# Performance work log

Hardware: AMD Instinct MI355X
Metric: run time of the kernel (lower is better)

Reference implementation:

```python
import jax, jax.numpy as jnp
import numpy as np

B, N, CIN, COUT = 8192, 17, 256, 256


def setup_inputs() -> dict:
    key = jax.random.key(0)
    k_x, k_w, k_m, k_a, k_b = jax.random.split(key, 5)
    stdv = 1.0 / np.sqrt(COUT)
    return {
        "x": jax.random.normal(k_x, (B, N, CIN), dtype=jnp.float32),
        # xavier_uniform with gain=1.414 ~ U(-a, a), a = gain*sqrt(6/(fan_in+fan_out))
        "W": jax.random.uniform(k_w, (2, CIN, COUT), dtype=jnp.float32,
                                minval=-1.0, maxval=1.0) * (1.414 * np.sqrt(6.0 / (CIN + COUT))),
        # M initialized to ones in torch; perturb slightly to exercise the math
        "M": 1.0 + 0.1 * jax.random.normal(k_m, (N, COUT), dtype=jnp.float32),
        "adj": jax.random.uniform(k_a, (N, N), dtype=jnp.float32),
        "adj2": jnp.full((N, N), 1e-6, dtype=jnp.float32),
        "bias": jax.random.uniform(k_b, (COUT,), dtype=jnp.float32,
                                   minval=-stdv, maxval=stdv),
    }


def reference(x, W, M, adj, adj2, bias):
    # x: [B, N, Cin], W: [2, Cin, Cout], M: [N, Cout], adj/adj2: [N, N]
    h0 = jnp.einsum("bnc,cd->bnd", x, W[0])  # [B, N, Cout]
    h1 = jnp.einsum("bnc,cd->bnd", x, W[1])  # [B, N, Cout]
    A = adj + adj2
    A = (A.T + A) * 0.5                       # symmetrize
    E = jnp.eye(A.shape[0], dtype=x.dtype)
    out = (jnp.einsum("ij,bjd->bid", A * E, M * h0)
           + jnp.einsum("ij,bjd->bid", A * (1.0 - E), M * h1))
    return out + bias[None, None, :]
```

## Files before the change

### kernel.cpp

```cpp
#include <hip/hip_runtime.h>
#include <hip/hip_bf16.h>

typedef float  f32x4  __attribute__((ext_vector_type(4)));
typedef __bf16 bf16x8 __attribute__((ext_vector_type(8)));
typedef short  s16x8  __attribute__((ext_vector_type(8)));
typedef short  s16x4  __attribute__((ext_vector_type(4)));

__device__ __forceinline__ short f2b(float f) {
  unsigned u = __builtin_bit_cast(unsigned, f);
  u = (u + 0x7fffu + ((u >> 16) & 1u)) >> 16;
  return (short)u;
}
__device__ __forceinline__ float b2f(short s) {
  unsigned u = ((unsigned)(unsigned short)s) << 16;
  return __builtin_bit_cast(float, u);
}
__device__ __forceinline__ s16x4 pack4(f32x4 a) {
  union { s16x4 v; __hip_bfloat162 h[2]; } u;
  u.h[0] = __float22bfloat162_rn(make_float2(a[0], a[1]));
  u.h[1] = __float22bfloat162_rn(make_float2(a[2], a[3]));
  return u.v;
}

__global__ void prep_wt(const float* __restrict__ W, short* __restrict__ Wt) {
  int q = blockIdx.x * blockDim.x + threadIdx.x;
  int mat = q >> 14;
  int rem = q & 16383;
  int d   = rem >> 6;
  int c4  = (rem & 63) << 2;
  const float* src = W + mat * 65536;
  s16x4 o;
  #pragma unroll
  for (int i = 0; i < 4; ++i) o[i] = f2b(src[(c4 + i) * 256 + d]);
  *(s16x4*)&Wt[q << 2] = o;
}

__global__ __launch_bounds__(256)
void fused_mgc(const float* __restrict__ x, const short* __restrict__ Wt,
               const float* __restrict__ M, const float* __restrict__ adj,
               const float* __restrict__ adj2, const float* __restrict__ bias,
               float* __restrict__ out) {
  __shared__ short smem[8976];
  __shared__ float aoff[289];
  __shared__ float diagl[17];

  const int tid  = threadIdx.x;
  const int lane = tid & 63;
  const int wv   = tid >> 6;
  const int m16  = lane & 15;
  const int qd   = lane >> 4;

  const int phys = blockIdx.x;
  const int xcd  = phys & 7;
  const int iseq = phys >> 3;
  const int bt   = xcd * 512 + (iseq >> 1);
  const int ct   = iseq & 1;

  for (int idx = tid; idx < 289; idx += 256) {
    int i = idx / 17, j = idx - i * 17;
    float v = 0.5f * ((adj[i*17+j] + adj2[i*17+j]) + (adj[j*17+i] + adj2[j*17+i]));
    aoff[idx] = (i == j) ? 0.0f : v;
    if (i == j) diagl[i] = adj[i*17+i] + adj2[i*17+i];
  }

  {
    const float* xbase = x + (size_t)bt * 34 * 256;
    const int c4 = (tid & 63) << 2;
    const int r0 = tid >> 6;
    #pragma unroll
    for (int it = 0; it < 9; ++it) {
      int row = r0 + it * 4;
      if (row < 34) {
        f32x4 v = *(const f32x4*)&xbase[row * 256 + c4];
        *(s16x4*)&smem[row * 264 + c4] = pack4(v);
      }
    }
  }

  f32x4 acc[3][4];
  #pragma unroll
  for (int a = 0; a < 3; ++a)
    #pragma unroll
    for (int b = 0; b < 4; ++b) acc[a][b] = (f32x4)0.0f;

  const short* wbase = Wt + (ct * 128 + wv * 32 + m16) * 256;

  __syncthreads();

  int arow[3];
  #pragma unroll
  for (int rf = 0; rf < 3; ++rf) {
    int r = rf * 16 + m16;
    arow[rf] = (r < 34 ? r : 33) * 264;
  }

  #pragma unroll
  for (int ks = 0; ks < 8; ++ks) {
    const int kq = ks * 32 + qd * 8;
    bf16x8 bfr[4];
    #pragma unroll
    for (int mc = 0; mc < 4; ++mc) {
      int mat = mc >> 1, cf = mc & 1;
      s16x8 t = *(const s16x8*)&wbase[mat * 65536 + cf * 4096 + kq];
      bfr[mc] = __builtin_bit_cast(bf16x8, t);
    }
    #pragma unroll
    for (int rf = 0; rf < 3; ++rf) {
      s16x8 t = *(const s16x8*)&smem[arow[rf] + kq];
      bf16x8 af = __builtin_bit_cast(bf16x8, t);
      #pragma unroll
      for (int mc = 0; mc < 4; ++mc)
        acc[rf][mc] = __builtin_amdgcn_mfma_f32_16x16x32_bf16(af, bfr[mc], acc[rf][mc], 0, 0, 0);
    }
  }

  __syncthreads();
  short* sbuf = smem;
  short* gbuf = smem + 4488;

  #pragma unroll
  for (int rf = 0; rf < 3; ++rf) {
    #pragma unroll
    for (int cf = 0; cf < 2; ++cf) {
      int c = wv * 32 + cf * 16 + m16;
      #pragma unroll
      for (int reg = 0; reg < 4; ++reg) {
        int r = rf * 16 + qd * 4 + reg;
        if (r < 34) {
          int n = r % 17;
          float mv = M[n * 256 + ct * 128 + c];
          sbuf[r * 132 + c] = f2b(diagl[n] * mv * acc[rf][cf][reg]);
          gbuf[r * 132 + c] = f2b(mv * acc[rf][2 + cf][reg]);
        }
      }
    }
  }
  __syncthreads();
  const int d7   = tid & 127;
  const int g    = tid >> 7;
  const float bi = bias[ct * 128 + d7];
  {
    int rbase = g * 17;
    float gr[17];
    #pragma unroll
    for (int j = 0; j < 17; ++j) gr[j] = b2f(gbuf[(rbase + j) * 132 + d7]);
    #pragma unroll
    for (int i = 0; i < 17; ++i) {
      float s = b2f(sbuf[(rbase + i) * 132 + d7]) + bi;
      #pragma unroll
      for (int j = 0; j < 17; ++j) s += aoff[i * 17 + j] * gr[j];
      out[((bt * 2 + g) * 17 + i) * 256 + ct * 128 + d7] = s;
    }
  }
}

extern "C" void kernel_launch(void* const* d_in, const int* in_sizes, int n_in,
                              void* d_out, int out_size, void* d_ws, size_t ws_size,
                              hipStream_t stream) {
  const float* x    = (const float*)d_in[0];
  const float* W    = (const float*)d_in[1];
  const float* M    = (const float*)d_in[2];
  const float* adj  = (const float*)d_in[3];
  const float* adj2 = (const float*)d_in[4];
  const float* bias = (const float*)d_in[5];
  float* out = (float*)d_out;
  short* Wt  = (short*)d_ws;

  prep_wt<<<128, 256, 0, stream>>>(W, Wt);
  fused_mgc<<<8192, 256, 0, stream>>>(x, Wt, M, adj, adj2, bias, out);
}
```

Measured before the change: 413.2 us.

## Loop each block over eight batch tiles with register prefetch of next x

Each block now processes eight consecutive batch tiles in a loop, so the grid shrinks by a factor of eight. The next tile's x is prefetched into registers during the current tile's MFMA and epilogue. M and the adjacency setup are staged into shared memory once per block. The aim is to hide global-load latency and amortise per-block setup, at the cost of more registers, fewer resident blocks and extra barriers per tile.

```diff
diff --git a/kernel.cpp b/kernel.cpp
--- a/kernel.cpp
+++ b/kernel.cpp
@@ -40,7 +40,8 @@
                const float* __restrict__ M, const float* __restrict__ adj,
                const float* __restrict__ adj2, const float* __restrict__ bias,
                float* __restrict__ out) {
-  __shared__ short smem[8976];
+  __shared__ short xs[8976];
+  __shared__ float ms[2176];
   __shared__ float aoff[289];
   __shared__ float diagl[17];
 
@@ -50,42 +51,36 @@
   const int m16  = lane & 15;
   const int qd   = lane >> 4;
 
-  const int phys = blockIdx.x;
-  const int xcd  = phys & 7;
-  const int iseq = phys >> 3;
-  const int bt   = xcd * 512 + (iseq >> 1);
-  const int ct   = iseq & 1;
+  const int phys   = blockIdx.x;
+  const int xcd    = phys & 7;
+  const int iseq   = phys >> 3;
+  const int ct     = iseq & 1;
+  const int btbase = (xcd * 64 + (iseq >> 1)) * 8;
 
+  const int c4 = (tid & 63) << 2;
+  const int r0 = tid >> 6;
+
+  f32x4 xp[9];
+  {
+    const float* xb = x + (size_t)btbase * 34 * 256;
+    #pragma unroll
+    for (int it = 0; it < 9; ++it) {
+      int row = r0 + it * 4;
+      if (row < 34) xp[it] = *(const f32x4*)&xb[row * 256 + c4];
+    }
+  }
   for (int idx = tid; idx < 289; idx += 256) {
     int i = idx / 17, j = idx - i * 17;
     float v = 0.5f * ((adj[i*17+j] + adj2[i*17+j]) + (adj[j*17+i] + adj2[j*17+i]));
     aoff[idx] = (i == j) ? 0.0f : v;
     if (i == j) diagl[i] = adj[i*17+i] + adj2[i*17+i];
   }
-
-  {
-    const float* xbase = x + (size_t)bt * 34 * 256;
-    const int c4 = (tid & 63) << 2;
-    const int r0 = tid >> 6;
-    #pragma unroll
-    for (int it = 0; it < 9; ++it) {
-      int row = r0 + it * 4;
-      if (row < 34) {
-        f32x4 v = *(const f32x4*)&xbase[row * 256 + c4];
-        *(s16x4*)&smem[row * 264 + c4] = pack4(v);
-      }
-    }
+  for (int q = tid; q < 544; q += 256) {
+    int n = q >> 5, cq = (q & 31) << 2;
+    *(f32x4*)&ms[n * 128 + cq] = *(const f32x4*)&M[n * 256 + ct * 128 + cq];
   }
 
-  f32x4 acc[3][4];
-  #pragma unroll
-  for (int a = 0; a < 3; ++a)
-    #pragma unroll
-    for (int b = 0; b < 4; ++b) acc[a][b] = (f32x4)0.0f;
-
   const short* wbase = Wt + (ct * 128 + wv * 32 + m16) * 256;
-
-  __syncthreads();
 
   int arow[3];
   #pragma unroll
@@ -94,63 +89,91 @@
     arow[rf] = (r < 34 ? r : 33) * 264;
   }
 
-  #pragma unroll
-  for (int ks = 0; ks < 8; ++ks) {
-    const int kq = ks * 32 + qd * 8;
-    bf16x8 bfr[4];
+  const int d7   = tid & 127;
+  const int g    = tid >> 7;
+  const float bi = bias[ct * 128 + d7];
+
+  for (int t = 0; t < 8; ++t) {
+    const int bt = btbase + t;
+
     #pragma unroll
-    for (int mc = 0; mc < 4; ++mc) {
-      int mat = mc >> 1, cf = mc & 1;
-      s16x8 t = *(const s16x8*)&wbase[mat * 65536 + cf * 4096 + kq];
-      bfr[mc] = __builtin_bit_cast(bf16x8, t);
+    for (int it = 0; it < 9; ++it) {
+      int row = r0 + it * 4;
+      if (row < 34) *(s16x4*)&xs[row * 264 + c4] = pack4(xp[it]);
     }
+    __syncthreads();
+
+    if (t < 7) {
+      const float* xb = x + (size_t)(bt + 1) * 34 * 256;
+      #pragma unroll
+      for (int it = 0; it < 9; ++it) {
+        int row = r0 + it * 4;
+        if (row < 34) xp[it] = *(const f32x4*)&xb[row * 256 + c4];
+      }
+    }
+
+    f32x4 acc[3][4];
+    #pragma unroll
+    for (int a = 0; a < 3; ++a)
+      #pragma unroll
+      for (int b = 0; b < 4; ++b) acc[a][b] = (f32x4)0.0f;
+
+    #pragma unroll
+    for (int ks = 0; ks < 8; ++ks) {
+      const int kq = ks * 32 + qd * 8;
+      bf16x8 bfr[4];
+      #pragma unroll
+      for (int mc = 0; mc < 4; ++mc) {
+        int mat = mc >> 1, cf = mc & 1;
+        s16x8 w = *(const s16x8*)&wbase[mat * 65536 + cf * 4096 + kq];
+        bfr[mc] = __builtin_bit_cast(bf16x8, w);
+      }
+      #pragma unroll
+      for (int rf = 0; rf < 3; ++rf) {
+        s16x8 a8 = *(const s16x8*)&xs[arow[rf] + kq];
+        bf16x8 af = __builtin_bit_cast(bf16x8, a8);
+        #pragma unroll
+        for (int mc = 0; mc < 4; ++mc)
+          acc[rf][mc] = __builtin_amdgcn_mfma_f32_16x16x32_bf16(af, bfr[mc], acc[rf][mc], 0, 0, 0);
+      }
+    }
+    __syncthreads();
+
+    short* sbuf = xs;
+    short* gbuf = xs + 4488;
     #pragma unroll
     for (int rf = 0; rf < 3; ++rf) {
-      s16x8 t = *(const s16x8*)&smem[arow[rf] + kq];
-      bf16x8 af = __builtin_bit_cast(bf16x8, t);
       #pragma unroll
-      for (int mc = 0; mc < 4; ++mc)
-        acc[rf][mc] = __builtin_amdgcn_mfma_f32_16x16x32_bf16(af, bfr[mc], acc[rf][mc], 0, 0, 0);
-    }
-  }
-
-  __syncthreads();
-  short* sbuf = smem;
-  short* gbuf = smem + 4488;
-
-  #pragma unroll
-  for (int rf = 0; rf < 3; ++rf) {
-    #pragma unroll
-    for (int cf = 0; cf < 2; ++cf) {
-      int c = wv * 32 + cf * 16 + m16;
-      #pragma unroll
-      for (int reg = 0; reg < 4; ++reg) {
-        int r = rf * 16 + qd * 4 + reg;
-        if (r < 34) {
-          int n = r % 17;
-          float mv = M[n * 256 + ct * 128 + c];
-          sbuf[r * 132 + c] = f2b(diagl[n] * mv * acc[rf][cf][reg]);
-          gbuf[r * 132 + c] = f2b(mv * acc[rf][2 + cf][reg]);
+      for (int cf = 0; cf < 2; ++cf) {
+        int c = wv * 32 + cf * 16 + m16;
+        #pragma unroll
+        for (int reg = 0; reg < 4; ++reg) {
+          int r = rf * 16 + qd * 4 + reg;
+          if (r < 34) {
+            int n = r - (r >= 17 ? 17 : 0);
+            float mv = ms[n * 128 + c];
+            sbuf[r * 132 + c] = f2b(diagl[n] * mv * acc[rf][cf][reg]);
+            gbuf[r * 132 + c] = f2b(mv * acc[rf][2 + cf][reg]);
+          }
         }
       }
     }
-  }
-  __syncthreads();
-  const int d7   = tid & 127;
-  const int g    = tid >> 7;
-  const float bi = bias[ct * 128 + d7];
-  {
-    int rbase = g * 17;
-    float gr[17];
-    #pragma unroll
-    for (int j = 0; j < 17; ++j) gr[j] = b2f(gbuf[(rbase + j) * 132 + d7]);
-    #pragma unroll
-    for (int i = 0; i < 17; ++i) {
-      float s = b2f(sbuf[(rbase + i) * 132 + d7]) + bi;
+    __syncthreads();
+
+    {
+      int rbase = g * 17;
+      float gr[17];
       #pragma unroll
-      for (int j = 0; j < 17; ++j) s += aoff[i * 17 + j] * gr[j];
-      out[((bt * 2 + g) * 17 + i) * 256 + ct * 128 + d7] = s;
+      for (int j = 0; j < 17; ++j) gr[j] = b2f(gbuf[(rbase + j) * 132 + d7]);
+      #pragma unroll
+      for (int i = 0; i < 17; ++i) {
+        float s = b2f(sbuf[(rbase + i) * 132 + d7]) + bi;
+        #pragma unroll
+        for (int j = 0; j < 17; ++j) s += aoff[i * 17 + j] * gr[j];
+        out[((bt * 2 + g) * 17 + i) * 256 + ct * 128 + d7] = s;
+      }
     }
+    __syncthreads();
   }
 }
 
@@ -167,5 +190,5 @@
   short* Wt  = (short*)d_ws;
 
   prep_wt<<<128, 256, 0, stream>>>(W, Wt);
-  fused_mgc<<<8192, 256, 0, stream>>>(x, Wt, M, adj, adj2, bias, out);
+  fused_mgc<<<1024, 256, 0, stream>>>(x, Wt, M, adj, adj2, bias, out);
 }
```

Result: faster. 366.3 us (-11.3%).

## Retile fused GCN kernel to 136-row blocks with 64 output columns each

Applied to the files above, without the earlier changes.

Each block now handles 8 batch items (136 rows) and a 64-column slice instead of 2 items and 128 columns. Each wave owns 34 rows and all 64 columns of both weight matrices, so weight fragments are shared across more rows. M is staged once in shared memory. The cost is that each x row is now loaded and converted by four column-tile blocks instead of two, and the block uses much more LDS, which may lower occupancy.

```diff
diff --git a/kernel.cpp b/kernel.cpp
--- a/kernel.cpp
+++ b/kernel.cpp
@@ -40,7 +40,8 @@
                const float* __restrict__ M, const float* __restrict__ adj,
                const float* __restrict__ adj2, const float* __restrict__ bias,
                float* __restrict__ out) {
-  __shared__ short smem[8976];
+  __shared__ short xs[35904];
+  __shared__ float ms[1088];
   __shared__ float aoff[289];
   __shared__ float diagl[17];
 
@@ -53,8 +54,8 @@
   const int phys = blockIdx.x;
   const int xcd  = phys & 7;
   const int iseq = phys >> 3;
-  const int bt   = xcd * 512 + (iseq >> 1);
-  const int ct   = iseq & 1;
+  const int bt   = xcd * 128 + (iseq >> 2);
+  const int ct   = iseq & 3;
 
   for (int idx = tid; idx < 289; idx += 256) {
     int i = idx / 17, j = idx - i * 17;
@@ -62,94 +63,102 @@
     aoff[idx] = (i == j) ? 0.0f : v;
     if (i == j) diagl[i] = adj[i*17+i] + adj2[i*17+i];
   }
+  for (int q = tid; q < 1088; q += 256) {
+    int n = q >> 6, c = q & 63;
+    ms[q] = M[n * 256 + ct * 64 + c];
+  }
 
   {
-    const float* xbase = x + (size_t)bt * 34 * 256;
+    const float* xbase = x + (size_t)bt * 136 * 256;
     const int c4 = (tid & 63) << 2;
     const int r0 = tid >> 6;
     #pragma unroll
-    for (int it = 0; it < 9; ++it) {
+    for (int it = 0; it < 34; ++it) {
       int row = r0 + it * 4;
-      if (row < 34) {
-        f32x4 v = *(const f32x4*)&xbase[row * 256 + c4];
-        *(s16x4*)&smem[row * 264 + c4] = pack4(v);
-      }
+      f32x4 v = *(const f32x4*)&xbase[row * 256 + c4];
+      *(s16x4*)&xs[row * 264 + c4] = pack4(v);
     }
   }
 
-  f32x4 acc[3][4];
+  f32x4 acc[3][8];
   #pragma unroll
   for (int a = 0; a < 3; ++a)
     #pragma unroll
-    for (int b = 0; b < 4; ++b) acc[a][b] = (f32x4)0.0f;
+    for (int b = 0; b < 8; ++b) acc[a][b] = (f32x4)0.0f;
 
-  const short* wbase = Wt + (ct * 128 + wv * 32 + m16) * 256;
+  const short* wbase = Wt + (ct * 64 + m16) * 256;
 
   __syncthreads();
 
   int arow[3];
   #pragma unroll
   for (int rf = 0; rf < 3; ++rf) {
-    int r = rf * 16 + m16;
-    arow[rf] = (r < 34 ? r : 33) * 264;
+    int r = wv * 34 + rf * 16 + m16;
+    arow[rf] = (r < 136 ? r : 135) * 264;
   }
 
   #pragma unroll
   for (int ks = 0; ks < 8; ++ks) {
     const int kq = ks * 32 + qd * 8;
-    bf16x8 bfr[4];
+    bf16x8 bfr[8];
     #pragma unroll
-    for (int mc = 0; mc < 4; ++mc) {
-      int mat = mc >> 1, cf = mc & 1;
-      s16x8 t = *(const s16x8*)&wbase[mat * 65536 + cf * 4096 + kq];
-      bfr[mc] = __builtin_bit_cast(bf16x8, t);
-    }
+    for (int mat = 0; mat < 2; ++mat)
+      #pragma unroll
+      for (int cfr = 0; cfr < 4; ++cfr) {
+        s16x8 w = *(const s16x8*)&wbase[mat * 65536 + cfr * 4096 + kq];
+        bfr[mat * 4 + cfr] = __builtin_bit_cast(bf16x8, w);
+      }
     #pragma unroll
     for (int rf = 0; rf < 3; ++rf) {
-      s16x8 t = *(const s16x8*)&smem[arow[rf] + kq];
-      bf16x8 af = __builtin_bit_cast(bf16x8, t);
+      s16x8 a8 = *(const s16x8*)&xs[arow[rf] + kq];
+      bf16x8 af = __builtin_bit_cast(bf16x8, a8);
       #pragma unroll
-      for (int mc = 0; mc < 4; ++mc)
-        acc[rf][mc] = __builtin_amdgcn_mfma_f32_16x16x32_bf16(af, bfr[mc], acc[rf][mc], 0, 0, 0);
+      for (int b = 0; b < 8; ++b)
+        acc[rf][b] = __builtin_amdgcn_mfma_f32_16x16x32_bf16(af, bfr[b], acc[rf][b], 0, 0, 0);
     }
   }
+  __syncthreads();
 
-  __syncthreads();
-  short* sbuf = smem;
-  short* gbuf = smem + 4488;
-
+  short* sbuf = xs;
+  short* gbuf = xs + 9248;
   #pragma unroll
   for (int rf = 0; rf < 3; ++rf) {
     #pragma unroll
-    for (int cf = 0; cf < 2; ++cf) {
-      int c = wv * 32 + cf * 16 + m16;
+    for (int cfr = 0; cfr < 4; ++cfr) {
+      int c = cfr * 16 + m16;
       #pragma unroll
       for (int reg = 0; reg < 4; ++reg) {
-        int r = rf * 16 + qd * 4 + reg;
-        if (r < 34) {
+        int rl = rf * 16 + qd * 4 + reg;
+        if (rl < 34) {
+          int r = wv * 34 + rl;
           int n = r % 17;
-          float mv = M[n * 256 + ct * 128 + c];
-          sbuf[r * 132 + c] = f2b(diagl[n] * mv * acc[rf][cf][reg]);
-          gbuf[r * 132 + c] = f2b(mv * acc[rf][2 + cf][reg]);
+          float mv = ms[n * 64 + c];
+          sbuf[r * 68 + c] = f2b(diagl[n] * mv * acc[rf][cfr][reg]);
+          gbuf[r * 68 + c] = f2b(mv * acc[rf][4 + cfr][reg]);
         }
       }
     }
   }
   __syncthreads();
-  const int d7   = tid & 127;
-  const int g    = tid >> 7;
-  const float bi = bias[ct * 128 + d7];
+
   {
-    int rbase = g * 17;
-    float gr[17];
+    const int d6 = tid & 63;
+    const int gq = tid >> 6;
+    const float bi = bias[ct * 64 + d6];
     #pragma unroll
-    for (int j = 0; j < 17; ++j) gr[j] = b2f(gbuf[(rbase + j) * 132 + d7]);
-    #pragma unroll
-    for (int i = 0; i < 17; ++i) {
-      float s = b2f(sbuf[(rbase + i) * 132 + d7]) + bi;
+    for (int gg = 0; gg < 2; ++gg) {
+      int g = gq * 2 + gg;
+      int rbase = g * 17;
+      float gr[17];
       #pragma unroll
-      for (int j = 0; j < 17; ++j) s += aoff[i * 17 + j] * gr[j];
-      out[((bt * 2 + g) * 17 + i) * 256 + ct * 128 + d7] = s;
+      for (int j = 0; j < 17; ++j) gr[j] = b2f(gbuf[(rbase + j) * 68 + d6]);
+      #pragma unroll
+      for (int i = 0; i < 17; ++i) {
+        float s = b2f(sbuf[(rbase + i) * 68 + d6]) + bi;
+        #pragma unroll
+        for (int j = 0; j < 17; ++j) s += aoff[i * 17 + j] * gr[j];
+        out[((size_t)(bt * 8 + g) * 17 + i) * 256 + ct * 64 + d6] = s;
+      }
     }
   }
 }
@@ -167,5 +176,5 @@
   short* Wt  = (short*)d_ws;
 
   prep_wt<<<128, 256, 0, stream>>>(W, Wt);
-  fused_mgc<<<8192, 256, 0, stream>>>(x, Wt, M, adj, adj2, bias, out);
+  fused_mgc<<<4096, 256, 0, stream>>>(x, Wt, M, adj, adj2, bias, out);
 }
```

Measured after the change: 774.7 us. 1.87x slower.
